# Optimization experiments

Hardware: AMD Instinct MI355X
Metric: run time of the kernel (lower is better)

The kernel has to match this reference:

```python
import jax, jax.numpy as jnp
import numpy as np

EMBED_DIM = 2048
N_HEADS = 16
HEAD_DIM = EMBED_DIM // N_HEADS  # 128
ROPE_BASE = 10000.0


def _rope(x):
    # x: (B, H, L, d) -- torchtune-style interleaved RoPE over position axis L
    L, d = x.shape[-2], x.shape[-1]
    inv_freq = 1.0 / (ROPE_BASE ** (jnp.arange(0, d, 2, dtype=jnp.float32) / d))  # (d/2,)
    freqs = jnp.arange(L, dtype=jnp.float32)[:, None] * inv_freq[None, :]          # (L, d/2)
    cos = jnp.cos(freqs).astype(x.dtype)
    sin = jnp.sin(freqs).astype(x.dtype)
    x1 = x[..., 0::2]  # (B,H,L,d/2)
    x2 = x[..., 1::2]
    out_even = x1 * cos - x2 * sin
    out_odd = x2 * cos + x1 * sin
    return jnp.stack([out_even, out_odd], axis=-1).reshape(x.shape)


def setup_inputs() -> dict:
    key = jax.random.key(0)
    ks = jax.random.split(key, 9)
    B, L, D = 64, 256, EMBED_DIM
    x = jax.random.normal(ks[0], (B, L, D), dtype=jnp.float32)
    s = 0.02
    wq = jax.random.normal(ks[1], (D, D), dtype=jnp.float32) * s
    wk = jax.random.normal(ks[2], (D, D), dtype=jnp.float32) * s
    wv = jax.random.normal(ks[3], (D, D), dtype=jnp.float32) * s
    wo = jax.random.normal(ks[4], (D, D), dtype=jnp.float32) * s
    bq = jax.random.normal(ks[5], (D,), dtype=jnp.float32) * s
    bk = jax.random.normal(ks[6], (D,), dtype=jnp.float32) * s
    bv = jax.random.normal(ks[7], (D,), dtype=jnp.float32) * s
    bo = jax.random.normal(ks[8], (D,), dtype=jnp.float32) * s
    return {"x": x, "wq": wq, "bq": bq, "wk": wk, "bk": bk,
            "wv": wv, "bv": bv, "wo": wo, "bo": bo}


def reference(x, wq, bq, wk, bk, wv, bv, wo, bo):
    B, L, D = x.shape
    H, hd = N_HEADS, HEAD_DIM

    def proj(w, b):
        y = jnp.einsum('bld,de->ble', x, w) + b
        return y.reshape(B, L, H, hd).transpose(0, 2, 1, 3)  # (B,H,L,hd)

    q = _rope(proj(wq, bq))
    k = _rope(proj(wk, bk))
    v = proj(wv, bv)

    scale = 1.0 / jnp.sqrt(jnp.asarray(hd, dtype=x.dtype))
    scores = jnp.einsum('bhqd,bhkd->bhqk', q, k) * scale  # (B,H,L,L)
    causal = jnp.tril(jnp.ones((L, L), dtype=bool))
    scores = jnp.where(causal[None, None], scores, -jnp.inf)
    attn = jax.nn.softmax(scores, axis=-1)
    out = jnp.einsum('bhqk,bhkd->bhqd', attn, v)  # (B,H,L,hd)
    out = out.transpose(0, 2, 1, 3).reshape(B, L, D)
    return jnp.einsum('bld,de->ble', out, wo) + bo
```

## Files before the change

### kernel.cpp

```cpp
#include <hip/hip_runtime.h>
#include <math.h>

typedef __bf16 bf16;
typedef float f32x4 __attribute__((ext_vector_type(4)));
typedef bf16  bf16x4 __attribute__((ext_vector_type(4)));
typedef bf16  bf16x8 __attribute__((ext_vector_type(8)));

#define N_B  64
#define N_L  256
#define N_H  16
#define N_D  2048
#define N_HD 128
#define M_TOT (N_B * N_L)

static __device__ __forceinline__ f32x4 shflx4(f32x4 v, int m) {
  f32x4 r;
  r[0] = __shfl_xor(v[0], m);
  r[1] = __shfl_xor(v[1], m);
  r[2] = __shfl_xor(v[2], m);
  r[3] = __shfl_xor(v[3], m);
  return r;
}
static __device__ __forceinline__ f32x4 max4(f32x4 a, f32x4 b) {
  f32x4 r;
  r[0] = fmaxf(a[0], b[0]); r[1] = fmaxf(a[1], b[1]);
  r[2] = fmaxf(a[2], b[2]); r[3] = fmaxf(a[3], b[3]);
  return r;
}

__global__ void k_cast_x(const float* __restrict__ x, bf16* __restrict__ xb, int n4) {
  int i = blockIdx.x * blockDim.x + threadIdx.x;
  int st = gridDim.x * blockDim.x;
  for (; i < n4; i += st) {
    float4 v = ((const float4*)x)[i];
    bf16x4 o;
    o[0] = (bf16)v.x; o[1] = (bf16)v.y; o[2] = (bf16)v.z; o[3] = (bf16)v.w;
    ((bf16x4*)xb)[i] = o;
  }
}

__global__ void k_transpose_w4(const float* __restrict__ w0, const float* __restrict__ w1,
                               const float* __restrict__ w2, const float* __restrict__ w3,
                               bf16* __restrict__ t0, bf16* __restrict__ t1,
                               bf16* __restrict__ t2, bf16* __restrict__ t3) {
  __shared__ float t[32][33];
  const float* w; bf16* wt;
  switch (blockIdx.z) {
    case 0:  w = w0; wt = t0; break;
    case 1:  w = w1; wt = t1; break;
    case 2:  w = w2; wt = t2; break;
    default: w = w3; wt = t3; break;
  }
  int n0 = blockIdx.x * 32, k0 = blockIdx.y * 32;
  t[threadIdx.y][threadIdx.x] = w[(size_t)(k0 + threadIdx.y) * N_D + n0 + threadIdx.x];
  __syncthreads();
  wt[(size_t)(n0 + threadIdx.y) * N_D + k0 + threadIdx.x] = (bf16)t[threadIdx.x][threadIdx.y];
}

__global__ void k_trig(float2* __restrict__ tab) {
  int idx = blockIdx.x * blockDim.x + threadIdx.x;
  if (idx < N_L * (N_HD / 2)) {
    int l = idx >> 6, i = idx & 63;
    float ang = (float)l * powf(10000.0f, -(float)(2 * i) / 128.0f);
    tab[idx].x = cosf(ang);
    tab[idx].y = sinf(ang);
  }
}


#define GLOAD(GP, LP) __builtin_amdgcn_global_load_lds( \
    (const __attribute__((address_space(1))) void*)(GP), \
    (__attribute__((address_space(3))) void*)(LP), 16, 0, 0)
#define BARR()  __builtin_amdgcn_s_barrier()
#define SCHED() __builtin_amdgcn_sched_barrier(0)
#define PRIO1() __builtin_amdgcn_s_setprio(1)
#define PRIO0() __builtin_amdgcn_s_setprio(0)
#define WAITLGKM4() asm volatile("s_waitcnt lgkmcnt(4)" ::: "memory")
#define WAITLGKM8() asm volatile("s_waitcnt lgkmcnt(8)" ::: "memory")
#define WAITVM4()   asm volatile("s_waitcnt vmcnt(4)" ::: "memory")
#define WAITVM6()   asm volatile("s_waitcnt vmcnt(6)" ::: "memory")

#define STAGE_A(X, KT, BUF) do { \
  GLOAD(Ag + (size_t)srcOffA[0][X] + (size_t)((KT) & 31) * 64, (BUF) + ldsOffA[0][X]); \
  GLOAD(Ag + (size_t)srcOffA[1][X] + (size_t)((KT) & 31) * 64, (BUF) + ldsOffA[1][X]); \
} while (0)
#define STAGE_B(X, KT, BUF) do { \
  GLOAD(Bg + (size_t)srcOffB[0][X] + (size_t)((KT) & 31) * 64, (BUF) + ldsOffB[0][X]); \
  GLOAD(Bg + (size_t)srcOffB[1][X] + (size_t)((KT) & 31) * 64, (BUF) + ldsOffB[1][X]); \
} while (0)

#define RD_A(DST, MH, KK, BUF) do { \
  _Pragma("unroll") for (int i_ = 0; i_ < 4; ++i_) { \
    const int R_ = wm * 128 + (MH) * 64 + i_ * 16 + lr; \
    DST[i_] = *(const bf16x8*)&(BUF)[R_ * 64 + ((((KK) * 4 + lg) ^ (R_ & 7)) << 3)]; \
  } \
} while (0)
#define RD_B(DST, KK, BUF) do { \
  _Pragma("unroll") for (int j_ = 0; j_ < 4; ++j_) { \
    const int R_ = wn * 64 + j_ * 16 + lr; \
    DST[j_] = *(const bf16x8*)&(BUF)[R_ * 64 + ((((KK) * 4 + lg) ^ (R_ & 7)) << 3)]; \
  } \
} while (0)

#define MFMA16(AB, BB, MH) do { \
  _Pragma("unroll") for (int i_ = 0; i_ < 4; ++i_) \
  _Pragma("unroll") for (int j_ = 0; j_ < 4; ++j_) \
    acc[(MH) * 4 + i_][j_] = __builtin_amdgcn_mfma_f32_16x16x32_bf16( \
        AB[i_], BB[j_], acc[(MH) * 4 + i_], [j_] + 0, 0, 0, 0); \
} while (0)
#undef MFMA16
#define MFMA16(AB, BB, MH) do { \
  _Pragma("unroll") for (int i_ = 0; i_ < 4; ++i_) \
  _Pragma("unroll") for (int j_ = 0; j_ < 4; ++j_) \
    acc[(MH) * 4 + i_][j_] = __builtin_amdgcn_mfma_f32_16x16x32_bf16( \
        AB[i_], BB[j_], acc[(MH) * 4 + i_][j_], 0, 0, 0); \
} while (0)

#define TILE(T, CURA, CURB, OTHA, OTHB) do { \
   \
  STAGE_B(1, (T) + 1, OTHB); \
  RD_A(A1b, 0, 1, CURA); RD_B(B1b, 1, CURB); \
  SCHED(); WAITLGKM8(); SCHED(); \
  PRIO1(); MFMA16(A0b, B0b, 0); PRIO0(); \
  SCHED(); WAITVM6(); BARR(); \
   \
  STAGE_A(1, (T) + 1, OTHA); \
  RD_A(A0b, 1, 0, CURA); \
  SCHED(); WAITLGKM4(); SCHED(); \
  PRIO1(); MFMA16(A1b, B1b, 0); PRIO0(); \
  SCHED(); BARR(); \
   \
  STAGE_A(0, (T) + 2, CURA); \
  RD_A(A1b, 1, 1, CURA); \
  SCHED(); WAITLGKM4(); SCHED(); \
  PRIO1(); MFMA16(A0b, B0b, 1); PRIO0(); \
  SCHED(); WAITVM4(); BARR(); \
   \
  STAGE_B(0, (T) + 2, CURB); \
  RD_A(A0b, 0, 0, OTHA); RD_B(B0b, 0, OTHB); \
  SCHED(); WAITLGKM8(); SCHED(); \
  PRIO1(); MFMA16(A1b, B1b, 1); PRIO0(); \
  SCHED(); BARR(); \
} while (0)

template<int MODE>
__global__ __launch_bounds__(512, 2) void k_gemm256(
    const bf16* __restrict__ A, const bf16* __restrict__ BT,
    const float* __restrict__ bias, void* __restrict__ dstv,
    const float2* __restrict__ tab)
{
  __shared__ bf16 lds[2][2][256 * 64];
  const int bid = blockIdx.x;
  const int xcd = bid & 7, idx = bid >> 3;
  const int bm = xcd * 8 + (idx >> 3), bn = idx & 7;
  const int m0 = bm * 256, n0 = bn * 256;
  const int tid = threadIdx.x;
  const int wave = tid >> 6, lane = tid & 63;
  const int wm = wave >> 2, wn = wave & 3;
  const int lr = lane & 15, lg = lane >> 4;
  const bf16* __restrict__ Ag = A;
  const bf16* __restrict__ Bg = BT;

  int srcOffA[2][2], srcOffB[2][2], ldsOffA[2][2], ldsOffB[2][2];
  {
    const int g7 = tid & 7;
#pragma unroll
    for (int u = 0; u < 2; ++u) {
      const int rl  = u * 64 + (tid >> 3);
      const int rl0 = u * 64 + wave * 8;
#pragma unroll
      for (int X = 0; X < 2; ++X) {
        const int rA  = ((rl >> 6) << 7)  | (X << 6) | (rl & 63);
        const int rA0 = ((rl0 >> 6) << 7) | (X << 6) | (rl0 & 63);
        srcOffA[u][X] = (m0 + rA) * N_D + ((g7 ^ (rA & 7)) << 3);
        ldsOffA[u][X] = rA0 * 64;
        const int rB  = ((rl >> 5) << 6)  | (X << 5) | (rl & 31);
        const int rB0 = ((rl0 >> 5) << 6) | (X << 5) | (rl0 & 31);
        srcOffB[u][X] = (n0 + rB) * N_D + ((g7 ^ (rB & 7)) << 3);
        ldsOffB[u][X] = rB0 * 64;
      }
    }
  }

  bf16* bufA0 = &lds[0][0][0];
  bf16* bufB0 = &lds[0][1][0];
  bf16* bufA1 = &lds[1][0][0];
  bf16* bufB1 = &lds[1][1][0];

  f32x4 acc[8][4];
#pragma unroll
  for (int i = 0; i < 8; ++i)
#pragma unroll
    for (int j = 0; j < 4; ++j)
      acc[i][j] = (f32x4){0.f, 0.f, 0.f, 0.f};

  bf16x8 A0b[4], A1b[4], B0b[4], B1b[4];

  STAGE_A(0, 0, bufA0); STAGE_B(0, 0, bufB0);
  STAGE_B(1, 0, bufB0); STAGE_A(1, 0, bufA0);
  STAGE_A(0, 1, bufA1); STAGE_B(0, 1, bufB1);
  SCHED(); WAITVM4(); BARR(); SCHED();
  RD_A(A0b, 0, 0, bufA0); RD_B(B0b, 0, bufB0);
  SCHED();

#pragma unroll 1
  for (int t = 0; t < N_D / 64; t += 2) {
    TILE(t,     bufA0, bufB0, bufA1, bufB1);
    TILE(t + 1, bufA1, bufB1, bufA0, bufB0);
  }

#pragma unroll
  for (int i = 0; i < 8; ++i) {
#pragma unroll
    for (int r = 0; r < 4; ++r) {
      const int m = m0 + wm * 128 + i * 16 + lg * 4 + r;
#pragma unroll
      for (int j = 0; j < 4; ++j) {
        const int n = n0 + wn * 64 + j * 16 + lr;
        float v = acc[i][j][r] + bias[n];
        if (MODE == 3) {
          float partner = __shfl_xor(v, 1);
          const int d = n & 127, l = m & 255;
          float2 cs = tab[(l << 6) | (d >> 1)];
          v = (d & 1) ? (v * cs.x + partner * cs.y) : (v * cs.x - partner * cs.y);
        }
        if (MODE == 0 || MODE == 3) {
          bf16* dst = (bf16*)dstv;
          const int b = m >> 8, l = m & 255;
          const int h = n >> 7, d = n & 127;
          dst[(((size_t)b * N_H + h) * N_L + l) * N_HD + d] = (bf16)v;
        } else if (MODE == 2) {
          bf16* dst = (bf16*)dstv;
          const int b = m >> 8, l = m & 255;
          const int h = n >> 7, d = n & 127;
          dst[(((size_t)b * N_H + h) * N_HD + d) * N_L + l] = (bf16)v;
        } else {
          float* dst = (float*)dstv;
          dst[(size_t)m * N_D + n] = v;
        }
      }
    }
  }
}

__global__ __launch_bounds__(512) void k_attn_mfma(
    const bf16* __restrict__ Q, const bf16* __restrict__ K,
    const bf16* __restrict__ Vt, bf16* __restrict__ O)
{
  __shared__ bf16 Kl[N_L * N_HD];
  __shared__ bf16 Pl[8][16][56];

  const int bh = blockIdx.x;
  const int b = bh >> 4, h = bh & 15;
  const int tid = threadIdx.x;
  const int wave = tid >> 6, lane = tid & 63;
  const int c = lane & 15, g8 = lane >> 4;

  const bf16* Qg = Q + (size_t)bh * (N_L * N_HD);
  const bf16* Kg = K + (size_t)bh * (N_L * N_HD);
  const bf16* Vg = Vt + (size_t)bh * (N_L * N_HD);

#pragma unroll
  for (int t = 0; t < 8; ++t) {
    int idx = tid + 512 * t;
    int row = idx >> 4, g = idx & 15;
    const bf16* src = Kg + row * N_HD + ((g ^ (row & 7)) << 3);
    __builtin_amdgcn_global_load_lds(
        (const __attribute__((address_space(1))) void*)src,
        (__attribute__((address_space(3))) void*)(Kl + (size_t)wave * 512 + (size_t)t * 4096),
        16, 0, 0);
  }
  __syncthreads();

  const float scale = 0.08838834764831843f;

  for (int half = 0; half < 2; ++half) {
    const int qb = half ? (15 - wave) : wave;
    const int q0 = qb * 16;

    bf16x8 qf[4];
#pragma unroll
    for (int dk = 0; dk < 4; ++dk)
      qf[dk] = *(const bf16x8*)(Qg + (size_t)(q0 + c) * N_HD + dk * 32 + g8 * 8);

    f32x4 o[8];
#pragma unroll
    for (int dj = 0; dj < 8; ++dj) o[dj] = (f32x4){0.f, 0.f, 0.f, 0.f};
    f32x4 mrow = (f32x4){-INFINITY, -INFINITY, -INFINITY, -INFINITY};
    f32x4 lrow = (f32x4){0.f, 0.f, 0.f, 0.f};

    const int nsteps = ((q0 + 15) >> 5) + 1;
    for (int js = 0; js < nsteps; ++js) {
      const int j0 = js * 32;

      bf16x8 vf[4];
#pragma unroll
      for (int dj = 0; dj < 4; ++dj)
        vf[dj] = *(const bf16x8*)(Vg + (size_t)(dj * 16 + c) * N_L + j0 + g8 * 8);

      f32x4 s0 = (f32x4){0.f, 0.f, 0.f, 0.f};
      f32x4 s1 = (f32x4){0.f, 0.f, 0.f, 0.f};
#pragma unroll
      for (int dk = 0; dk < 4; ++dk) {
        int row0 = j0 + c;
        int row1 = j0 + 16 + c;
        bf16x8 kf0 = *(const bf16x8*)(Kl + row0 * N_HD + (((dk * 4 + g8) ^ (row0 & 7)) << 3));
        bf16x8 kf1 = *(const bf16x8*)(Kl + row1 * N_HD + (((dk * 4 + g8) ^ (row1 & 7)) << 3));
        s0 = __builtin_amdgcn_mfma_f32_16x16x32_bf16(qf[dk], kf0, s0, 0, 0, 0);
        s1 = __builtin_amdgcn_mfma_f32_16x16x32_bf16(qf[dk], kf1, s1, 0, 0, 0);
      }

      f32x4 sv0, sv1;
#pragma unroll
      for (int r = 0; r < 4; ++r) { sv0[r] = s0[r] * scale; sv1[r] = s1[r] * scale; }
      if (j0 + 31 > q0) {
#pragma unroll
        for (int r = 0; r < 4; ++r) {
          int q = q0 + g8 * 4 + r;
          if (j0 + c > q)      sv0[r] = -INFINITY;
          if (j0 + 16 + c > q) sv1[r] = -INFINITY;
        }
      }

      f32x4 mx = max4(sv0, sv1);
      mx = max4(mx, shflx4(mx, 1));
      mx = max4(mx, shflx4(mx, 2));
      mx = max4(mx, shflx4(mx, 4));
      mx = max4(mx, shflx4(mx, 8));
      f32x4 mnew = max4(mrow, mx);
      f32x4 resc, p0, p1;
#pragma unroll
      for (int r = 0; r < 4; ++r) {
        resc[r] = __expf(mrow[r] - mnew[r]);
        p0[r] = __expf(sv0[r] - mnew[r]);
        p1[r] = __expf(sv1[r] - mnew[r]);
      }
      f32x4 rsum = p0 + p1;
      rsum += shflx4(rsum, 1);
      rsum += shflx4(rsum, 2);
      rsum += shflx4(rsum, 4);
      rsum += shflx4(rsum, 8);
      lrow = lrow * resc + rsum;
      mrow = mnew;
#pragma unroll
      for (int dj = 0; dj < 8; ++dj) o[dj] *= resc;

#pragma unroll
      for (int r = 0; r < 4; ++r) {
        Pl[wave][g8 * 4 + r][c] = (bf16)p0[r];
        Pl[wave][g8 * 4 + r][16 + c] = (bf16)p1[r];
      }
      bf16x8 pf = *(const bf16x8*)&Pl[wave][c][g8 * 8];

      bf16x8 vg[4];
#pragma unroll
      for (int dj = 0; dj < 4; ++dj)
        vg[dj] = *(const bf16x8*)(Vg + (size_t)((dj + 4) * 16 + c) * N_L + j0 + g8 * 8);

#pragma unroll
      for (int dj = 0; dj < 4; ++dj)
        o[dj] = __builtin_amdgcn_mfma_f32_16x16x32_bf16(pf, vf[dj], o[dj], 0, 0, 0);
#pragma unroll
      for (int dj = 0; dj < 4; ++dj)
        o[dj + 4] = __builtin_amdgcn_mfma_f32_16x16x32_bf16(pf, vg[dj], o[dj + 4], 0, 0, 0);
    }

    f32x4 inv;
#pragma unroll
    for (int r = 0; r < 4; ++r) inv[r] = 1.0f / lrow[r];
#pragma unroll
    for (int dj = 0; dj < 8; ++dj) {
      f32x4 ov = o[dj] * inv;
#pragma unroll
      for (int r = 0; r < 4; ++r) {
        int q = q0 + g8 * 4 + r;
        int d = dj * 16 + c;
        O[(((size_t)b * N_L + q) * N_H + h) * N_HD + d] = (bf16)ov[r];
      }
    }
  }
}

extern "C" void kernel_launch(void* const* d_in, const int* in_sizes, int n_in,
                              void* d_out, int out_size, void* d_ws, size_t ws_size,
                              hipStream_t stream) {
  const float* x  = (const float*)d_in[0];
  const float* wq = (const float*)d_in[1];
  const float* bq = (const float*)d_in[2];
  const float* wk = (const float*)d_in[3];
  const float* bk = (const float*)d_in[4];
  const float* wv = (const float*)d_in[5];
  const float* bv = (const float*)d_in[6];
  const float* wo = (const float*)d_in[7];
  const float* bo = (const float*)d_in[8];

  char* ws = (char*)d_ws;
  const size_t WSZ = (size_t)N_D * N_D * sizeof(bf16);
  const size_t XSZ = (size_t)M_TOT * N_D * sizeof(bf16);
  bf16* wqT = (bf16*)(ws);
  bf16* wkT = (bf16*)(ws + WSZ);
  bf16* wvT = (bf16*)(ws + 2 * WSZ);
  bf16* woT = (bf16*)(ws + 3 * WSZ);
  bf16* xb  = (bf16*)(ws + 4 * WSZ);
  bf16* Qb  = (bf16*)(ws + 4 * WSZ + XSZ);
  bf16* Kb  = (bf16*)(ws + 4 * WSZ + 2 * XSZ);
  bf16* Vb  = (bf16*)(ws + 4 * WSZ + 3 * XSZ);
  bf16* Ob  = (bf16*)(ws + 4 * WSZ + 4 * XSZ);
  float2* tab = (float2*)(ws + 4 * WSZ + 5 * XSZ);

  k_cast_x<<<2048, 256, 0, stream>>>(x, xb, M_TOT * N_D / 4);
  dim3 tb(32, 32), tg(64, 64, 4);
  k_transpose_w4<<<tg, tb, 0, stream>>>(wq, wk, wv, wo, wqT, wkT, wvT, woT);
  k_trig<<<64, 256, 0, stream>>>(tab);

  const int grid = (M_TOT / 256) * (N_D / 256);
  k_gemm256<3><<<grid, 512, 0, stream>>>(xb, wqT, bq, Qb, tab);
  k_gemm256<3><<<grid, 512, 0, stream>>>(xb, wkT, bk, Kb, tab);
  k_gemm256<2><<<grid, 512, 0, stream>>>(xb, wvT, bv, Vb, tab);

  k_attn_mfma<<<1024, 512, 0, stream>>>(Qb, Kb, Vb, Ob);
  k_gemm256<1><<<grid, 512, 0, stream>>>(Ob, woT, bo, d_out, tab);
}
```

Before: 671.2 us.

## Fuse Q, K and V projection GEMMs into one launch with concatenated weights

Replaces three separate projection GEMM launches with a single 1536-block launch over a concatenated N dimension of 6144. This relies on wqT, wkT and wvT being contiguous in the workspace, and a new kernel concatenates the three biases. The epilogue picks RoPE plus the Q/K layout or the transposed V layout from the column range, relying on Q, K and V buffers also being contiguous. The aim is to cut launch overhead and tail effects and to improve scheduling across XCDs, at the cost of an extra small kernel and a divide/modulo in the block mapping.

```diff
diff --git a/kernel.cpp b/kernel.cpp
--- a/kernel.cpp
+++ b/kernel.cpp
@@ -67,6 +67,14 @@
   }
 }
 
+__global__ void k_concat_bias(const float* __restrict__ bq, const float* __restrict__ bk,
+                              const float* __restrict__ bv, float* __restrict__ out) {
+  int i = blockIdx.x * blockDim.x + threadIdx.x;
+  if (i < N_D)           out[i] = bq[i];
+  else if (i < 2 * N_D)  out[i] = bk[i - N_D];
+  else if (i < 3 * N_D)  out[i] = bv[i - 2 * N_D];
+}
+
 
 #define GLOAD(GP, LP) __builtin_amdgcn_global_load_lds( \
     (const __attribute__((address_space(1))) void*)(GP), \
@@ -102,13 +110,6 @@
   } \
 } while (0)
 
-#define MFMA16(AB, BB, MH) do { \
-  _Pragma("unroll") for (int i_ = 0; i_ < 4; ++i_) \
-  _Pragma("unroll") for (int j_ = 0; j_ < 4; ++j_) \
-    acc[(MH) * 4 + i_][j_] = __builtin_amdgcn_mfma_f32_16x16x32_bf16( \
-        AB[i_], BB[j_], acc[(MH) * 4 + i_], [j_] + 0, 0, 0, 0); \
-} while (0)
-#undef MFMA16
 #define MFMA16(AB, BB, MH) do { \
   _Pragma("unroll") for (int i_ = 0; i_ < 4; ++i_) \
   _Pragma("unroll") for (int j_ = 0; j_ < 4; ++j_) \
@@ -152,7 +153,9 @@
   __shared__ bf16 lds[2][2][256 * 64];
   const int bid = blockIdx.x;
   const int xcd = bid & 7, idx = bid >> 3;
-  const int bm = xcd * 8 + (idx >> 3), bn = idx & 7;
+  int bm, bn;
+  if (MODE == 4) { bm = xcd * 8 + idx / 24; bn = idx % 24; }
+  else           { bm = xcd * 8 + (idx >> 3); bn = idx & 7; }
   const int m0 = bm * 256, n0 = bn * 256;
   const int tid = threadIdx.x;
   const int wave = tid >> 6, lane = tid & 63;
@@ -218,22 +221,22 @@
       for (int j = 0; j < 4; ++j) {
         const int n = n0 + wn * 64 + j * 16 + lr;
         float v = acc[i][j][r] + bias[n];
-        if (MODE == 3) {
-          float partner = __shfl_xor(v, 1);
-          const int d = n & 127, l = m & 255;
-          float2 cs = tab[(l << 6) | (d >> 1)];
-          v = (d & 1) ? (v * cs.x + partner * cs.y) : (v * cs.x - partner * cs.y);
-        }
-        if (MODE == 0 || MODE == 3) {
+        if (MODE == 4) {
+          const int t = n >> 11;
+          const int nn = n & 2047;
+          const int b = m >> 8, l = m & 255;
+          const int h = nn >> 7, d = nn & 127;
           bf16* dst = (bf16*)dstv;
-          const int b = m >> 8, l = m & 255;
-          const int h = n >> 7, d = n & 127;
-          dst[(((size_t)b * N_H + h) * N_L + l) * N_HD + d] = (bf16)v;
-        } else if (MODE == 2) {
-          bf16* dst = (bf16*)dstv;
-          const int b = m >> 8, l = m & 255;
-          const int h = n >> 7, d = n & 127;
-          dst[(((size_t)b * N_H + h) * N_HD + d) * N_L + l] = (bf16)v;
+          if (t < 2) {
+            float partner = __shfl_xor(v, 1);
+            float2 cs = tab[(l << 6) | (d >> 1)];
+            v = (d & 1) ? (v * cs.x + partner * cs.y) : (v * cs.x - partner * cs.y);
+            dst[(size_t)t * M_TOT * N_D +
+                (((size_t)b * N_H + h) * N_L + l) * N_HD + d] = (bf16)v;
+          } else {
+            dst[(size_t)2 * M_TOT * N_D +
+                (((size_t)b * N_H + h) * N_HD + d) * N_L + l] = (bf16)v;
+          }
         } else {
           float* dst = (float*)dstv;
           dst[(size_t)m * N_D + n] = v;
@@ -407,17 +410,18 @@
   bf16* Vb  = (bf16*)(ws + 4 * WSZ + 3 * XSZ);
   bf16* Ob  = (bf16*)(ws + 4 * WSZ + 4 * XSZ);
   float2* tab = (float2*)(ws + 4 * WSZ + 5 * XSZ);
+  float* biasQKV = (float*)(ws + 4 * WSZ + 5 * XSZ + (size_t)N_L * 64 * sizeof(float2));
 
   k_cast_x<<<2048, 256, 0, stream>>>(x, xb, M_TOT * N_D / 4);
   dim3 tb(32, 32), tg(64, 64, 4);
   k_transpose_w4<<<tg, tb, 0, stream>>>(wq, wk, wv, wo, wqT, wkT, wvT, woT);
   k_trig<<<64, 256, 0, stream>>>(tab);
+  k_concat_bias<<<24, 256, 0, stream>>>(bq, bk, bv, biasQKV);
+
+  k_gemm256<4><<<1536, 512, 0, stream>>>(xb, wqT, biasQKV, Qb, tab);
+
+  k_attn_mfma<<<1024, 512, 0, stream>>>(Qb, Kb, Vb, Ob);
 
   const int grid = (M_TOT / 256) * (N_D / 256);
-  k_gemm256<3><<<grid, 512, 0, stream>>>(xb, wqT, bq, Qb, tab);
-  k_gemm256<3><<<grid, 512, 0, stream>>>(xb, wkT, bk, Kb, tab);
-  k_gemm256<2><<<grid, 512, 0, stream>>>(xb, wvT, bv, Vb, tab);
-
-  k_attn_mfma<<<1024, 512, 0, stream>>>(Qb, Kb, Vb, Ob);
   k_gemm256<1><<<grid, 512, 0, stream>>>(Ob, woT, bo, d_out, tab);
 }
```

Result: slower. 777.6 us (+15.9%).
